# Kernel tuning notes

Measured on AMD Instinct MI355X. Metric: run time of the kernel, lower is better.

Reference implementation:

```python
import jax, jax.numpy as jnp
import numpy as np

D = 768
H = 16
DK = D // H
DFF = 3072
POOL = 100
NCLS = 7
EPS = 1e-6


def layer_norm(x, a, b):
    # torch: (x - mean) / (std + eps), std unbiased (ddof=1)
    mean = jnp.mean(x, axis=-1, keepdims=True)
    var = jnp.sum((x - mean) ** 2, axis=-1, keepdims=True) / (x.shape[-1] - 1)
    return a * (x - mean) / (jnp.sqrt(var) + EPS) + b


def mha(x, Wq, bq, Wk, bk, Wv, bv, Wo, bo):
    B, S, _ = x.shape
    def split(h):
        return h.reshape(B, S, H, DK).transpose(0, 2, 1, 3)  # [B,H,S,DK]
    q = split(x @ Wq + bq)
    k = split(x @ Wk + bk)
    v = split(x @ Wv + bv)
    scores = jnp.einsum('bhqd,bhkd->bhqk', q, k) / jnp.sqrt(jnp.float32(DK))
    p = jax.nn.softmax(scores, axis=-1)
    o = jnp.einsum('bhqk,bhkd->bhqd', p, v)
    o = o.transpose(0, 2, 1, 3).reshape(B, S, D)
    return o @ Wo + bo


def setup_inputs() -> dict:
    key = jax.random.key(0)
    ks = jax.random.split(key, 24)
    B, S = 8, 1023
    s = 0.02
    inp = {
        'text_features': jax.random.normal(ks[0], (B, S, D), jnp.float32),
        'prompt_pool': jax.random.normal(ks[1], (POOL, D), jnp.float32),
        'cls_token': jax.random.normal(ks[2], (1, 1, D), jnp.float32),
        'Wq': jax.random.normal(ks[3], (D, D), jnp.float32) * s,
        'bq': jnp.zeros((D,), jnp.float32),
        'Wk': jax.random.normal(ks[4], (D, D), jnp.float32) * s,
        'bk': jnp.zeros((D,), jnp.float32),
        'Wv': jax.random.normal(ks[5], (D, D), jnp.float32) * s,
        'bv': jnp.zeros((D,), jnp.float32),
        'Wo': jax.random.normal(ks[6], (D, D), jnp.float32) * s,
        'bo': jnp.zeros((D,), jnp.float32),
        'ln1_a': jnp.ones((D,), jnp.float32),
        'ln1_b': jnp.zeros((D,), jnp.float32),
        'ln2_a': jnp.ones((D,), jnp.float32),
        'ln2_b': jnp.zeros((D,), jnp.float32),
        'W1': jax.random.normal(ks[7], (D, DFF), jnp.float32) * s,
        'b1': jnp.zeros((DFF,), jnp.float32),
        'W2': jax.random.normal(ks[8], (DFF, D), jnp.float32) * s,
        'b2': jnp.zeros((D,), jnp.float32),
        'lnf_a': jnp.ones((D,), jnp.float32),
        'lnf_b': jnp.zeros((D,), jnp.float32),
        'Wpool': jax.random.normal(ks[9], (D, POOL), jnp.float32) * s,
        'bpool': jnp.zeros((POOL,), jnp.float32),
        'Wcls': jax.random.normal(ks[10], (D, NCLS), jnp.float32) * s,
        'bcls': jnp.zeros((NCLS,), jnp.float32),
    }
    return inp


def reference(text_features, prompt_pool, cls_token, Wq, bq, Wk, bk, Wv, bv, Wo, bo,
              ln1_a, ln1_b, ln2_a, ln2_b, W1, b1, W2, b2, lnf_a, lnf_b,
              Wpool, bpool, Wcls, bcls):
    B = text_features.shape[0]
    x = jnp.concatenate([jnp.broadcast_to(cls_token, (B, 1, D)), text_features], axis=1)
    # EncoderLayer (N=1), dropout in eval mode (identity)
    x = x + mha(layer_norm(x, ln1_a, ln1_b), Wq, bq, Wk, bk, Wv, bv, Wo, bo)
    h = layer_norm(x, ln2_a, ln2_b)
    x = x + (jax.nn.relu(h @ W1 + b1) @ W2 + b2)
    x = layer_norm(x, lnf_a, lnf_b)
    cls = x[:, 0, :]  # [B, D]
    probabilities = jax.nn.softmax(cls @ Wpool + bpool, axis=1)  # [B, POOL]
    class_logits = cls @ Wcls + bcls  # [B, NCLS]
    class_probs = jax.nn.softmax(class_logits, axis=1)
    entropy = -jnp.sum(class_probs * jnp.log(class_probs + 1e-9), axis=1)
    max_entropy = jnp.log(jnp.float32(7.0))
    norm_ent = entropy / max_entropy
    adjusted_k = jnp.clip(jnp.floor(1.0 + norm_ent * (POOL - 1)).astype(jnp.int32), 1, POOL)  # [B]
    # full descending top-k (jit-friendly: pad to POOL instead of data-dependent max_k)
    _, top_idx = jax.lax.top_k(probabilities, POOL)  # [B, POOL]
    gathered = prompt_pool[top_idx]  # [B, POOL, D]
    keep = (jnp.arange(POOL)[None, :] < adjusted_k[:, None]).astype(prompt_pool.dtype)
    selected_prompts = gathered * keep[:, :, None]
    return (selected_prompts, class_logits)
```

## Files before the change

### kernel.cpp

```cpp
#include <hip/hip_runtime.h>


#define OUT_CLS_OFF 614400

__device__ __forceinline__ float bsum256(float v, float* red) {
    int lane = threadIdx.x & 63, w = threadIdx.x >> 6;
#pragma unroll
    for (int off = 1; off < 64; off <<= 1) v += __shfl_xor(v, off);
    __syncthreads();
    if (lane == 0) red[w] = v;
    __syncthreads();
    return red[0] + red[1] + red[2] + red[3];
}
__device__ __forceinline__ float bmax256(float v, float* red) {
    int lane = threadIdx.x & 63, w = threadIdx.x >> 6;
#pragma unroll
    for (int off = 1; off < 64; off <<= 1) v = fmaxf(v, __shfl_xor(v, off));
    __syncthreads();
    if (lane == 0) red[w] = v;
    __syncthreads();
    return fmaxf(fmaxf(red[0], red[1]), fmaxf(red[2], red[3]));
}

__global__ __launch_bounds__(256) void q0_gemv(
    const float* __restrict__ clsT, const float* __restrict__ ga,
    const float* __restrict__ gb, const float* __restrict__ Wq,
    const float* __restrict__ bq, float* __restrict__ q0)
{
    __shared__ float ys[768];
    __shared__ float red[4];
    __shared__ float4 part[16][17];
    int t = threadIdx.x;
    float a0 = clsT[t], a1 = clsT[t + 256], a2 = clsT[t + 512];
    float mean = bsum256(a0 + a1 + a2, red) * (1.0f / 768.0f);
    float d0 = a0 - mean, d1 = a1 - mean, d2 = a2 - mean;
    float var = bsum256(d0 * d0 + d1 * d1 + d2 * d2, red) * (1.0f / 767.0f);
    float den = sqrtf(var) + 1e-6f;
    ys[t]       = (ga[t] * d0) / den + gb[t];
    ys[t + 256] = (ga[t + 256] * d1) / den + gb[t + 256];
    ys[t + 512] = (ga[t + 512] * d2) / den + gb[t + 512];
    __syncthreads();
    int c = blockIdx.x * 64 + (t & 15) * 4;
    int kq = t >> 4;
    float4 acc = {0.f, 0.f, 0.f, 0.f};
#pragma unroll 8
    for (int i = 0; i < 48; ++i) {
        int k = kq * 48 + i;
        float4 w = *(const float4*)&Wq[(size_t)k * 768 + c];
        float y = ys[k];
        acc.x = fmaf(y, w.x, acc.x); acc.y = fmaf(y, w.y, acc.y);
        acc.z = fmaf(y, w.z, acc.z); acc.w = fmaf(y, w.w, acc.w);
    }
    part[kq][t & 15] = acc;
    __syncthreads();
    if (t < 16) {
        float4 s = {0.f, 0.f, 0.f, 0.f};
#pragma unroll
        for (int i = 0; i < 16; ++i) {
            float4 v = part[i][t];
            s.x += v.x; s.y += v.y; s.z += v.z; s.w += v.w;
        }
        int cc = blockIdx.x * 64 + t * 4;
        float4 b4 = *(const float4*)&bq[cc];
        q0[cc] = s.x + b4.x; q0[cc + 1] = s.y + b4.y;
        q0[cc + 2] = s.z + b4.z; q0[cc + 3] = s.w + b4.w;
    }
}

__global__ __launch_bounds__(256) void wkq_prep(
    const float* __restrict__ Wk, const float* __restrict__ bk,
    const float* __restrict__ q0, float* __restrict__ wkqc)
{
    __shared__ float qs[768];
    int t = threadIdx.x;
    qs[t] = q0[t]; qs[t + 256] = q0[t + 256]; qs[t + 512] = q0[t + 512];
    __syncthreads();
    const float invs = 0.14433756729740643f;
    int kl = t >> 4, h = t & 15;
    int k = blockIdx.x * 16 + kl;
    const float* wr = Wk + (size_t)k * 768 + h * 48;
    const float* qh = qs + h * 48;
    float a = 0.f;
#pragma unroll
    for (int d = 0; d < 48; d += 4) {
        float4 w = *(const float4*)&wr[d];
        a += w.x * qh[d] + w.y * qh[d + 1] + w.z * qh[d + 2] + w.w * qh[d + 3];
    }
    wkqc[k * 16 + h] = a * invs;
    if (blockIdx.x == 0 && t < 16) {
        float c = 0.f;
        for (int d = 0; d < 48; ++d) c += bk[t * 48 + d] * qs[t * 48 + d];
        wkqc[12288 + t] = c * invs;
    }
}

__global__ __launch_bounds__(256) void wkq_consts(
    const float* __restrict__ ga, const float* __restrict__ gb,
    float* __restrict__ wkqc)
{
    __shared__ float pA[16][17], pB[16][17];
    int t = threadIdx.x;
    int h = t & 15, dg = t >> 4;
    float a = 0.f, bs = 0.f;
#pragma unroll 8
    for (int i = 0; i < 48; ++i) {
        int d = dg * 48 + i;
        float wv = wkqc[d * 16 + h];
        a = fmaf(ga[d], wv, a);
        bs = fmaf(gb[d], wv, bs);
    }
    pA[dg][h] = a; pB[dg][h] = bs;
    __syncthreads();
    if (t < 16) {
        float sa = 0.f, sb = 0.f;
#pragma unroll
        for (int i = 0; i < 16; ++i) { sa += pA[i][t]; sb += pB[i][t]; }
        wkqc[12304 + t] = sa;
        wkqc[12320 + t] = sb + wkqc[12288 + t];
    }
}

__global__ __launch_bounds__(256) void ln_scores(
    const float* __restrict__ tf, const float* __restrict__ clsT,
    const float* __restrict__ ga, const float* __restrict__ wkqc,
    float* __restrict__ sc, float2* __restrict__ stats)
{
    __shared__ float tr[256][17];
    __shared__ float partw[4][16];
    __shared__ float red[2][4][2];
    int t = threadIdx.x;
    int l = t & 63, w = t >> 6;

    float wk0[16], wk1[16], wk2[16];
    {
        const float4* p0 = (const float4*)(wkqc + t * 16);
        const float4* p1 = (const float4*)(wkqc + (t + 256) * 16);
        const float4* p2 = (const float4*)(wkqc + (t + 512) * 16);
#pragma unroll
        for (int q = 0; q < 4; ++q) {
            float4 v0 = p0[q], v1 = p1[q], v2 = p2[q];
            wk0[q * 4] = v0.x; wk0[q * 4 + 1] = v0.y; wk0[q * 4 + 2] = v0.z; wk0[q * 4 + 3] = v0.w;
            wk1[q * 4] = v1.x; wk1[q * 4 + 1] = v1.y; wk1[q * 4 + 2] = v1.z; wk1[q * 4 + 3] = v1.w;
            wk2[q * 4] = v2.x; wk2[q * 4 + 1] = v2.y; wk2[q * 4 + 2] = v2.z; wk2[q * 4 + 3] = v2.w;
        }
    }
    float ga0 = ga[t], ga1 = ga[t + 256], ga2 = ga[t + 512];
    float Sg = wkqc[12304 + (t & 15)];
    float Cg = wkqc[12320 + (t & 15)];

    int r0 = blockIdx.x * 8;
    for (int r = 0; r < 8; ++r) {
        int row = r0 + r;
        int b = row >> 10, j = row & 1023;
        const float* src = j ? (tf + ((size_t)b * 1023 + (j - 1)) * 768) : clsT;
        float x0 = src[t], x1 = src[t + 256], x2 = src[t + 512];
        float s1 = x0 + x1 + x2;
        float s2 = fmaf(x0, x0, fmaf(x1, x1, x2 * x2));
        float g0 = ga0 * x0, g1 = ga1 * x1, g2 = ga2 * x2;
        float dt[16];
#pragma unroll
        for (int h = 0; h < 16; ++h)
            dt[h] = fmaf(g0, wk0[h], fmaf(g1, wk1[h], g2 * wk2[h]));
#pragma unroll
        for (int off = 1; off < 64; off <<= 1) {
            s1 += __shfl_xor(s1, off);
            s2 += __shfl_xor(s2, off);
        }
        if (l == 0) { red[r & 1][w][0] = s1; red[r & 1][w][1] = s2; }
#pragma unroll
        for (int h = 0; h < 16; ++h) tr[t][h] = dt[h];
        __syncthreads();
        int hh = t & 15, ch = t >> 4;
        float v = 0.f;
#pragma unroll
        for (int i = 0; i < 16; ++i) v += tr[ch * 16 + i][hh];
        v += __shfl_xor(v, 16);
        v += __shfl_xor(v, 32);
        if (l < 16) partw[w][l] = v;
        __syncthreads();
        if (t < 16) {
            float dtot = partw[0][t] + partw[1][t] + partw[2][t] + partw[3][t];
            float s1t = red[r & 1][0][0] + red[r & 1][1][0] + red[r & 1][2][0] + red[r & 1][3][0];
            float s2t = red[r & 1][0][1] + red[r & 1][1][1] + red[r & 1][2][1] + red[r & 1][3][1];
            float mean = s1t * (1.0f / 768.0f);
            float var = (s2t - mean * s1t) * (1.0f / 767.0f);
            float rden = 1.0f / (sqrtf(var) + 1e-6f);
            float sv = rden * (dtot - mean * Sg) + Cg;
            sc[(((size_t)b * 16 + t) << 10) + j] = sv;
            if (t == 0) stats[row] = make_float2(mean, rden);
        }
    }
}

__global__ __launch_bounds__(256) void softmax_k(
    const float* __restrict__ sc, float* __restrict__ p)
{
    __shared__ float red[4];
    int bh = blockIdx.x, t = threadIdx.x;
    const float4* s4 = (const float4*)(sc + ((size_t)bh << 10));
    float4 v = s4[t];
    float m = fmaxf(fmaxf(v.x, v.y), fmaxf(v.z, v.w));
    float M = bmax256(m, red);
    float e0 = expf(v.x - M), e1 = expf(v.y - M), e2 = expf(v.z - M), e3 = expf(v.w - M);
    float Z = bsum256(e0 + e1 + e2 + e3, red);
    float4 o; o.x = e0 / Z; o.y = e1 / Z; o.z = e2 / Z; o.w = e3 / Z;
    ((float4*)(p + ((size_t)bh << 10)))[t] = o;
}

__global__ __launch_bounds__(256) void upart_k(
    const float* __restrict__ tf, const float* __restrict__ clsT,
    const float2* __restrict__ stats, const float* __restrict__ ga,
    const float* __restrict__ gb, const float* __restrict__ p,
    float* __restrict__ up)
{
    __shared__ float ps[16][32];
    int b = blockIdx.x & 7, jc = blockIdx.x >> 3;
    int t = threadIdx.x;
    if (t < 128) {
        int h = t >> 3, j4 = (t & 7) * 4;
        const float* prow = p + (((size_t)b * 16 + h) << 10) + jc * 32 + j4;
        float4 pv = *(const float4*)prow;
        ps[h][j4] = pv.x; ps[h][j4 + 1] = pv.y; ps[h][j4 + 2] = pv.z; ps[h][j4 + 3] = pv.w;
    }
    __syncthreads();
    float ga0 = ga[t], ga1 = ga[t + 256], ga2 = ga[t + 512];
    float gb0 = gb[t], gb1 = gb[t + 256], gb2 = gb[t + 512];
    float acc[16][3];
#pragma unroll
    for (int h = 0; h < 16; ++h) { acc[h][0] = 0.f; acc[h][1] = 0.f; acc[h][2] = 0.f; }

    int j0 = jc * 32;
    const float* s0p = j0 ? (tf + ((size_t)b * 1023 + (j0 - 1)) * 768) : clsT;
    float nx0 = s0p[t], nx1 = s0p[t + 256], nx2 = s0p[t + 512];
    float2 nst = stats[(b << 10) + j0];

    for (int jj = 0; jj < 32; ++jj) {
        float x0 = nx0, x1 = nx1, x2 = nx2;
        float2 st = nst;
        if (jj < 31) {
            int j2 = j0 + jj + 1;
            const float* sp = tf + ((size_t)b * 1023 + (j2 - 1)) * 768;
            nx0 = sp[t]; nx1 = sp[t + 256]; nx2 = sp[t + 512];
            nst = stats[(b << 10) + j2];
        }
        float xl0 = (ga0 * (x0 - st.x)) * st.y + gb0;
        float xl1 = (ga1 * (x1 - st.x)) * st.y + gb1;
        float xl2 = (ga2 * (x2 - st.x)) * st.y + gb2;
#pragma unroll
        for (int h = 0; h < 16; ++h) {
            float ph = ps[h][jj];
            acc[h][0] = fmaf(ph, xl0, acc[h][0]);
            acc[h][1] = fmaf(ph, xl1, acc[h][1]);
            acc[h][2] = fmaf(ph, xl2, acc[h][2]);
        }
    }
    float* o = up + (((size_t)b * 32 + jc) * 16) * 768;
#pragma unroll
    for (int h = 0; h < 16; ++h) {
        o[h * 768 + t] = acc[h][0];
        o[h * 768 + t + 256] = acc[h][1];
        o[h * 768 + t + 512] = acc[h][2];
    }
}

__global__ __launch_bounds__(256) void o0_k(
    const float* __restrict__ up, const float* __restrict__ Wv,
    const float* __restrict__ bv, float* __restrict__ o0)
{
    __shared__ float us[768];
    __shared__ float part[4][64];
    int h = blockIdx.x, b = blockIdx.y, t = threadIdx.x;
    float s0 = 0.f, s1 = 0.f, s2 = 0.f;
#pragma unroll 8
    for (int jc = 0; jc < 32; ++jc) {
        const float* q = up + (((size_t)b * 32 + jc) * 16 + h) * 768;
        s0 += q[t]; s1 += q[t + 256]; s2 += q[t + 512];
    }
    us[t] = s0; us[t + 256] = s1; us[t + 512] = s2;
    __syncthreads();
    int dd = t & 63, kg = t >> 6;
    float a = 0.f;
    if (dd < 48) {
#pragma unroll 8
        for (int i = 0; i < 192; ++i) {
            int k = kg * 192 + i;
            a = fmaf(us[k], Wv[(size_t)k * 768 + h * 48 + dd], a);
        }
    }
    part[kg][dd] = a;
    __syncthreads();
    if (t < 48)
        o0[(size_t)b * 768 + h * 48 + t] =
            part[0][t] + part[1][t] + part[2][t] + part[3][t] + bv[h * 48 + t];
}

__global__ __launch_bounds__(256) void x2_k(
    const float* __restrict__ o0, const float* __restrict__ Wo,
    const float* __restrict__ bo, const float* __restrict__ clsT,
    float* __restrict__ x2w)
{
    __shared__ float ys[768];
    __shared__ float4 part[16][17];
    int b = blockIdx.y, t = threadIdx.x;
    const float* xr = o0 + (size_t)b * 768;
    ys[t] = xr[t]; ys[t + 256] = xr[t + 256]; ys[t + 512] = xr[t + 512];
    __syncthreads();
    int c = blockIdx.x * 64 + (t & 15) * 4;
    int kq = t >> 4;
    float4 acc = {0.f, 0.f, 0.f, 0.f};
#pragma unroll 8
    for (int i = 0; i < 48; ++i) {
        int k = kq * 48 + i;
        float4 w = *(const float4*)&Wo[(size_t)k * 768 + c];
        float y = ys[k];
        acc.x = fmaf(y, w.x, acc.x); acc.y = fmaf(y, w.y, acc.y);
        acc.z = fmaf(y, w.z, acc.z); acc.w = fmaf(y, w.w, acc.w);
    }
    part[kq][t & 15] = acc;
    __syncthreads();
    if (t < 16) {
        float4 s = {0.f, 0.f, 0.f, 0.f};
#pragma unroll
        for (int i = 0; i < 16; ++i) {
            float4 v = part[i][t];
            s.x += v.x; s.y += v.y; s.z += v.z; s.w += v.w;
        }
        int cc = blockIdx.x * 64 + t * 4;
        float4 b4 = *(const float4*)&bo[cc];
        float4 r4 = *(const float4*)&clsT[cc];
        float* o = x2w + (size_t)b * 768 + cc;
        o[0] = s.x + b4.x + r4.x; o[1] = s.y + b4.y + r4.y;
        o[2] = s.z + b4.z + r4.z; o[3] = s.w + b4.w + r4.w;
    }
}

__global__ __launch_bounds__(256) void f1_k(
    const float* __restrict__ x2w, const float* __restrict__ ga,
    const float* __restrict__ gb, const float* __restrict__ W1,
    const float* __restrict__ b1, float* __restrict__ f1w)
{
    __shared__ float ys[768];
    __shared__ float red[4];
    __shared__ float4 part[8][33];
    int b = blockIdx.y, t = threadIdx.x;
    const float* xr = x2w + (size_t)b * 768;
    float a0 = xr[t], a1 = xr[t + 256], a2 = xr[t + 512];
    float mean = bsum256(a0 + a1 + a2, red) * (1.0f / 768.0f);
    float d0 = a0 - mean, d1 = a1 - mean, d2 = a2 - mean;
    float var = bsum256(d0 * d0 + d1 * d1 + d2 * d2, red) * (1.0f / 767.0f);
    float den = sqrtf(var) + 1e-6f;
    ys[t]       = (ga[t] * d0) / den + gb[t];
    ys[t + 256] = (ga[t + 256] * d1) / den + gb[t + 256];
    ys[t + 512] = (ga[t + 512] * d2) / den + gb[t + 512];
    __syncthreads();
    int c = blockIdx.x * 128 + (t & 31) * 4;
    int kq = t >> 5;
    float4 acc = {0.f, 0.f, 0.f, 0.f};
#pragma unroll 8
    for (int i = 0; i < 96; ++i) {
        int k = kq * 96 + i;
        float4 w = *(const float4*)&W1[(size_t)k * 3072 + c];
        float y = ys[k];
        acc.x = fmaf(y, w.x, acc.x); acc.y = fmaf(y, w.y, acc.y);
        acc.z = fmaf(y, w.z, acc.z); acc.w = fmaf(y, w.w, acc.w);
    }
    part[kq][t & 31] = acc;
    __syncthreads();
    if (t < 32) {
        float4 s = {0.f, 0.f, 0.f, 0.f};
#pragma unroll
        for (int i = 0; i < 8; ++i) {
            float4 v = part[i][t];
            s.x += v.x; s.y += v.y; s.z += v.z; s.w += v.w;
        }
        int cc = blockIdx.x * 128 + t * 4;
        float4 b4 = *(const float4*)&b1[cc];
        float* o = f1w + (size_t)b * 3072 + cc;
        o[0] = fmaxf(s.x + b4.x, 0.f); o[1] = fmaxf(s.y + b4.y, 0.f);
        o[2] = fmaxf(s.z + b4.z, 0.f); o[3] = fmaxf(s.w + b4.w, 0.f);
    }
}

__global__ __launch_bounds__(256) void x3_k(
    const float* __restrict__ f1w, const float* __restrict__ W2,
    const float* __restrict__ b2, const float* __restrict__ x2w,
    float* __restrict__ x3w)
{
    __shared__ float ys[3072];
    __shared__ float4 part[16][17];
    int b = blockIdx.y, t = threadIdx.x;
    const float* xr = f1w + (size_t)b * 3072;
    for (int i = t; i < 3072; i += 256) ys[i] = xr[i];
    __syncthreads();
    int c = blockIdx.x * 64 + (t & 15) * 4;
    int kq = t >> 4;
    float4 acc = {0.f, 0.f, 0.f, 0.f};
#pragma unroll 8
    for (int i = 0; i < 192; ++i) {
        int k = kq * 192 + i;
        float4 w = *(const float4*)&W2[(size_t)k * 768 + c];
        float y = ys[k];
        acc.x = fmaf(y, w.x, acc.x); acc.y = fmaf(y, w.y, acc.y);
        acc.z = fmaf(y, w.z, acc.z); acc.w = fmaf(y, w.w, acc.w);
    }
    part[kq][t & 15] = acc;
    __syncthreads();
    if (t < 16) {
        float4 s = {0.f, 0.f, 0.f, 0.f};
#pragma unroll
        for (int i = 0; i < 16; ++i) {
            float4 v = part[i][t];
            s.x += v.x; s.y += v.y; s.z += v.z; s.w += v.w;
        }
        int cc = blockIdx.x * 64 + t * 4;
        float4 b4 = *(const float4*)&b2[cc];
        const float* x2r = x2w + (size_t)b * 768 + cc;
        float* o = x3w + (size_t)b * 768 + cc;
        o[0] = x2r[0] + s.x + b4.x; o[1] = x2r[1] + s.y + b4.y;
        o[2] = x2r[2] + s.z + b4.z; o[3] = x2r[3] + s.w + b4.w;
    }
}

__global__ __launch_bounds__(256) void logits_part(
    const float* __restrict__ x3w, const float* __restrict__ ga,
    const float* __restrict__ gb, const float* __restrict__ Wpool,
    const float* __restrict__ Wcls, double* __restrict__ lp)
{
    __shared__ float ys[768];
    __shared__ float red[4];
    int kg = blockIdx.x, b = blockIdx.y, t = threadIdx.x;
    const float* xr = x3w + (size_t)b * 768;
    float a0 = xr[t], a1 = xr[t + 256], a2 = xr[t + 512];
    float mean = bsum256(a0 + a1 + a2, red) * (1.0f / 768.0f);
    float d0 = a0 - mean, d1 = a1 - mean, d2 = a2 - mean;
    float var = bsum256(d0 * d0 + d1 * d1 + d2 * d2, red) * (1.0f / 767.0f);
    float den = sqrtf(var) + 1e-6f;
    ys[t]       = (ga[t] * d0) / den + gb[t];
    ys[t + 256] = (ga[t + 256] * d1) / den + gb[t + 256];
    ys[t + 512] = (ga[t + 512] * d2) / den + gb[t + 512];
    __syncthreads();
    int kbase = kg * 96;
    if (t < 100) {
        double a = 0.0;
#pragma unroll 8
        for (int i = 0; i < 96; ++i) {
            int k = kbase + i;
            a = fma((double)ys[k], (double)Wpool[k * 100 + t], a);
        }
        lp[((size_t)b * 8 + kg) * 112 + t] = a;
    } else if (t < 107) {
        int c = t - 100;
        double a = 0.0;
#pragma unroll 8
        for (int i = 0; i < 96; ++i) {
            int k = kbase + i;
            a = fma((double)ys[k], (double)Wcls[k * 7 + c], a);
        }
        lp[((size_t)b * 8 + kg) * 112 + t] = a;
    }
}

__global__ __launch_bounds__(128) void head_decide(
    const double* __restrict__ lp, const float* __restrict__ bpool,
    const float* __restrict__ bcls, float* __restrict__ out,
    int* __restrict__ topw, int* __restrict__ kkw)
{
    __shared__ double sP[100];
    __shared__ double sC7[7];
    int b = blockIdx.x, t = threadIdx.x;
    if (t < 107) {
        double a = (t < 100) ? (double)bpool[t] : (double)bcls[t - 100];
#pragma unroll
        for (int kg = 0; kg < 8; ++kg) a += lp[((size_t)b * 8 + kg) * 112 + t];
        if (t < 100) sP[t] = a;
        else {
            sC7[t - 100] = a;
            out[OUT_CLS_OFF + b * 7 + (t - 100)] = (float)a;
        }
    }
    __syncthreads();
    double mx = sP[0];
    for (int j = 1; j < 100; ++j) mx = fmax(mx, sP[j]);
    double e = (t < 100) ? exp(sP[t] - mx) : 0.0;
    __syncthreads();
    if (t < 100) sP[t] = e;
    __syncthreads();
    double zs = 0.0;
    for (int j = 0; j < 100; ++j) zs += sP[j];
    __syncthreads();
    if (t < 100) sP[t] = e / zs;
    __syncthreads();
    if (t == 0) {
        double m7 = sC7[0];
        for (int j = 1; j < 7; ++j) m7 = fmax(m7, sC7[j]);
        double es[7]; double z = 0.0;
        for (int j = 0; j < 7; ++j) { es[j] = exp(sC7[j] - m7); z += es[j]; }
        double ent = 0.0;
        for (int j = 0; j < 7; ++j) { double pr = es[j] / z; ent -= pr * log(pr + 1e-9); }
        double ne = ent / log(7.0);
        int kk = (int)floor(1.0 + ne * 99.0);
        kkw[b] = kk < 1 ? 1 : (kk > 100 ? 100 : kk);
    }
    if (t < 100) {
        double pi = sP[t];
        int r = 0;
        for (int j = 0; j < 100; ++j) {
            double pj = sP[j];
            r += (pj > pi) || (pj == pi && j < t);
        }
        topw[b * 100 + r] = t;
    }
}

__global__ __launch_bounds__(192) void gather_k(
    const float* __restrict__ pool, const int* __restrict__ topw,
    const int* __restrict__ kkw, float* __restrict__ out)
{
    int r = blockIdx.x, b = blockIdx.y, t = threadIdx.x;
    int idx = topw[b * 100 + r];
    bool keep = r < kkw[b];
    const float4* src = (const float4*)(pool + (size_t)idx * 768);
    float4* dst = (float4*)(out + (size_t)b * 76800 + (size_t)r * 768);
    float4 z = {0.f, 0.f, 0.f, 0.f};
    dst[t] = keep ? src[t] : z;
}

extern "C" void kernel_launch(void* const* d_in, const int* in_sizes, int n_in,
                              void* d_out, int out_size, void* d_ws, size_t ws_size,
                              hipStream_t stream) {
    (void)in_sizes; (void)n_in; (void)out_size; (void)ws_size;
    const float* tf    = (const float*)d_in[0];
    const float* pool  = (const float*)d_in[1];
    const float* clsT  = (const float*)d_in[2];
    const float* Wq    = (const float*)d_in[3];
    const float* bq    = (const float*)d_in[4];
    const float* Wk    = (const float*)d_in[5];
    const float* bk    = (const float*)d_in[6];
    const float* Wv    = (const float*)d_in[7];
    const float* bv    = (const float*)d_in[8];
    const float* Wo    = (const float*)d_in[9];
    const float* bo    = (const float*)d_in[10];
    const float* ln1a  = (const float*)d_in[11];
    const float* ln1b  = (const float*)d_in[12];
    const float* ln2a  = (const float*)d_in[13];
    const float* ln2b  = (const float*)d_in[14];
    const float* W1    = (const float*)d_in[15];
    const float* b1    = (const float*)d_in[16];
    const float* W2    = (const float*)d_in[17];
    const float* b2    = (const float*)d_in[18];
    const float* lnfa  = (const float*)d_in[19];
    const float* lnfb  = (const float*)d_in[20];
    const float* Wpool = (const float*)d_in[21];
    const float* bpool = (const float*)d_in[22];
    const float* Wcls  = (const float*)d_in[23];
    const float* bcls  = (const float*)d_in[24];
    float* out = (float*)d_out;
    char* ws = (char*)d_ws;

    float*  sc    = (float*)(ws + 0);
    float*  p     = (float*)(ws + 524288);
    float2* stats = (float2*)(ws + 1048576);
    float*  wkqc  = (float*)(ws + 1114112);
    float*  q0    = (float*)(ws + 1163520);
    float*  upart = (float*)(ws + 1166592);
    float*  o0    = (float*)(ws + 13749504);
    float*  x2w   = (float*)(ws + 13774080);
    float*  f1w   = (float*)(ws + 13798656);
    float*  x3w   = (float*)(ws + 13896960);
    int*    topw  = (int*)(ws + 13921536);
    int*    kkw   = (int*)(ws + 13924736);
    double* lp    = (double*)(ws + 13924768);

    q0_gemv<<<12, 256, 0, stream>>>(clsT, ln1a, ln1b, Wq, bq, q0);
    wkq_prep<<<48, 256, 0, stream>>>(Wk, bk, q0, wkqc);
    wkq_consts<<<1, 256, 0, stream>>>(ln1a, ln1b, wkqc);
    ln_scores<<<1024, 256, 0, stream>>>(tf, clsT, ln1a, wkqc, sc, stats);
    softmax_k<<<128, 256, 0, stream>>>(sc, p);
    upart_k<<<256, 256, 0, stream>>>(tf, clsT, stats, ln1a, ln1b, p, upart);
    o0_k<<<dim3(16, 8), 256, 0, stream>>>(upart, Wv, bv, o0);
    x2_k<<<dim3(12, 8), 256, 0, stream>>>(o0, Wo, bo, clsT, x2w);
    f1_k<<<dim3(24, 8), 256, 0, stream>>>(x2w, ln2a, ln2b, W1, b1, f1w);
    x3_k<<<dim3(12, 8), 256, 0, stream>>>(f1w, W2, b2, x2w, x3w);
    logits_part<<<dim3(8, 8), 256, 0, stream>>>(x3w, lnfa, lnfb, Wpool, Wcls, lp);
    head_decide<<<8, 128, 0, stream>>>(lp, bpool, bcls, out, topw, kkw);
    gather_k<<<dim3(100, 8), 192, 0, stream>>>(pool, topw, kkw, out);
}
```

Baseline: 111.0 us.

## Fuse post-prep pipeline into one cooperative kernel with grid syncs

Replaces the chain of eleven kernels after the query prep with a single cooperative kernel of 256 blocks that runs each stage and separates them with grid.sync(). The aim is to remove per-launch overhead and tail gaps between many small kernels. It also folds the wkq_consts step into the prep kernels by precomputing ga·Wk and gb·Wk column sums, and prefetches the next row in the score and accumulation loops. In exchange the grid is limited to 256 blocks, so the row-heavy score stage does 32 rows per block instead of 8, and the large shared-memory footprint may limit occupancy.

New measurement: 365.0 us. 229% more time.

```diff
diff --git a/kernel.cpp b/kernel.cpp
--- a/kernel.cpp
+++ b/kernel.cpp
@@ -1,4 +1,7 @@
 #include <hip/hip_runtime.h>
+#include <hip/hip_cooperative_groups.h>
+
+namespace cg = cooperative_groups;
 
 
 #define OUT_CLS_OFF 614400
@@ -22,54 +25,88 @@
     return fmaxf(fmaxf(red[0], red[1]), fmaxf(red[2], red[3]));
 }
 
-__global__ __launch_bounds__(256) void q0_gemv(
+__global__ __launch_bounds__(256) void prep_a(
     const float* __restrict__ clsT, const float* __restrict__ ga,
     const float* __restrict__ gb, const float* __restrict__ Wq,
-    const float* __restrict__ bq, float* __restrict__ q0)
+    const float* __restrict__ bq, const float* __restrict__ Wk,
+    float* __restrict__ q0, float* __restrict__ colw)
 {
     __shared__ float ys[768];
     __shared__ float red[4];
-    __shared__ float4 part[16][17];
+    __shared__ float4 partA[16][17];
+    __shared__ float4 partB[16][17];
     int t = threadIdx.x;
-    float a0 = clsT[t], a1 = clsT[t + 256], a2 = clsT[t + 512];
-    float mean = bsum256(a0 + a1 + a2, red) * (1.0f / 768.0f);
-    float d0 = a0 - mean, d1 = a1 - mean, d2 = a2 - mean;
-    float var = bsum256(d0 * d0 + d1 * d1 + d2 * d2, red) * (1.0f / 767.0f);
-    float den = sqrtf(var) + 1e-6f;
-    ys[t]       = (ga[t] * d0) / den + gb[t];
-    ys[t + 256] = (ga[t + 256] * d1) / den + gb[t + 256];
-    ys[t + 512] = (ga[t + 512] * d2) / den + gb[t + 512];
-    __syncthreads();
-    int c = blockIdx.x * 64 + (t & 15) * 4;
-    int kq = t >> 4;
-    float4 acc = {0.f, 0.f, 0.f, 0.f};
-#pragma unroll 8
-    for (int i = 0; i < 48; ++i) {
-        int k = kq * 48 + i;
-        float4 w = *(const float4*)&Wq[(size_t)k * 768 + c];
-        float y = ys[k];
-        acc.x = fmaf(y, w.x, acc.x); acc.y = fmaf(y, w.y, acc.y);
-        acc.z = fmaf(y, w.z, acc.z); acc.w = fmaf(y, w.w, acc.w);
-    }
-    part[kq][t & 15] = acc;
-    __syncthreads();
-    if (t < 16) {
-        float4 s = {0.f, 0.f, 0.f, 0.f};
-#pragma unroll
-        for (int i = 0; i < 16; ++i) {
-            float4 v = part[i][t];
-            s.x += v.x; s.y += v.y; s.z += v.z; s.w += v.w;
-        }
-        int cc = blockIdx.x * 64 + t * 4;
-        float4 b4 = *(const float4*)&bq[cc];
-        q0[cc] = s.x + b4.x; q0[cc + 1] = s.y + b4.y;
-        q0[cc + 2] = s.z + b4.z; q0[cc + 3] = s.w + b4.w;
+    if (blockIdx.x < 12) {
+        float a0 = clsT[t], a1 = clsT[t + 256], a2 = clsT[t + 512];
+        float mean = bsum256(a0 + a1 + a2, red) * (1.0f / 768.0f);
+        float d0 = a0 - mean, d1 = a1 - mean, d2 = a2 - mean;
+        float var = bsum256(d0 * d0 + d1 * d1 + d2 * d2, red) * (1.0f / 767.0f);
+        float den = sqrtf(var) + 1e-6f;
+        ys[t]       = (ga[t] * d0) / den + gb[t];
+        ys[t + 256] = (ga[t + 256] * d1) / den + gb[t + 256];
+        ys[t + 512] = (ga[t + 512] * d2) / den + gb[t + 512];
+        __syncthreads();
+        int c = blockIdx.x * 64 + (t & 15) * 4;
+        int kq = t >> 4;
+        float4 acc = {0.f, 0.f, 0.f, 0.f};
+#pragma unroll 8
+        for (int i = 0; i < 48; ++i) {
+            int k = kq * 48 + i;
+            float4 w = *(const float4*)&Wq[(size_t)k * 768 + c];
+            float y = ys[k];
+            acc.x = fmaf(y, w.x, acc.x); acc.y = fmaf(y, w.y, acc.y);
+            acc.z = fmaf(y, w.z, acc.z); acc.w = fmaf(y, w.w, acc.w);
+        }
+        partA[kq][t & 15] = acc;
+        __syncthreads();
+        if (t < 16) {
+            float4 s = {0.f, 0.f, 0.f, 0.f};
+#pragma unroll
+            for (int i = 0; i < 16; ++i) {
+                float4 v = partA[i][t];
+                s.x += v.x; s.y += v.y; s.z += v.z; s.w += v.w;
+            }
+            int cc = blockIdx.x * 64 + t * 4;
+            float4 b4 = *(const float4*)&bq[cc];
+            q0[cc] = s.x + b4.x; q0[cc + 1] = s.y + b4.y;
+            q0[cc + 2] = s.z + b4.z; q0[cc + 3] = s.w + b4.w;
+        }
+    } else {
+        int c = (blockIdx.x - 12) * 64 + (t & 15) * 4;
+        int kq = t >> 4;
+        float4 aa = {0.f, 0.f, 0.f, 0.f}, ab = {0.f, 0.f, 0.f, 0.f};
+#pragma unroll 8
+        for (int i = 0; i < 48; ++i) {
+            int k = kq * 48 + i;
+            float4 w = *(const float4*)&Wk[(size_t)k * 768 + c];
+            float g = ga[k], h = gb[k];
+            aa.x = fmaf(g, w.x, aa.x); aa.y = fmaf(g, w.y, aa.y);
+            aa.z = fmaf(g, w.z, aa.z); aa.w = fmaf(g, w.w, aa.w);
+            ab.x = fmaf(h, w.x, ab.x); ab.y = fmaf(h, w.y, ab.y);
+            ab.z = fmaf(h, w.z, ab.z); ab.w = fmaf(h, w.w, ab.w);
+        }
+        partA[kq][t & 15] = aa;
+        partB[kq][t & 15] = ab;
+        __syncthreads();
+        if (t < 16) {
+            float4 sa = {0.f, 0.f, 0.f, 0.f}, sb = {0.f, 0.f, 0.f, 0.f};
+#pragma unroll
+            for (int i = 0; i < 16; ++i) {
+                float4 va = partA[i][t], vb = partB[i][t];
+                sa.x += va.x; sa.y += va.y; sa.z += va.z; sa.w += va.w;
+                sb.x += vb.x; sb.y += vb.y; sb.z += vb.z; sb.w += vb.w;
+            }
+            int cc = (blockIdx.x - 12) * 64 + t * 4;
+            *(float4*)&colw[cc] = sa;
+            *(float4*)&colw[768 + cc] = sb;
+        }
     }
 }
 
-__global__ __launch_bounds__(256) void wkq_prep(
+__global__ __launch_bounds__(256) void prep_b(
     const float* __restrict__ Wk, const float* __restrict__ bk,
-    const float* __restrict__ q0, float* __restrict__ wkqc)
+    const float* __restrict__ q0, const float* __restrict__ colw,
+    float* __restrict__ wkqc)
 {
     __shared__ float qs[768];
     int t = threadIdx.x;
@@ -88,51 +125,56 @@
     }
     wkqc[k * 16 + h] = a * invs;
     if (blockIdx.x == 0 && t < 16) {
-        float c = 0.f;
-        for (int d = 0; d < 48; ++d) c += bk[t * 48 + d] * qs[t * 48 + d];
-        wkqc[12288 + t] = c * invs;
+        float cd = 0.f, sa = 0.f, sb = 0.f;
+        for (int d = 0; d < 48; ++d) {
+            int dd = t * 48 + d;
+            cd = fmaf(bk[dd], qs[dd], cd);
+            sa = fmaf(colw[dd], qs[dd], sa);
+            sb = fmaf(colw[768 + dd], qs[dd], sb);
+        }
+        wkqc[12304 + t] = sa * invs;
+        wkqc[12320 + t] = sb * invs + cd * invs;
     }
 }
 
-__global__ __launch_bounds__(256) void wkq_consts(
-    const float* __restrict__ ga, const float* __restrict__ gb,
-    float* __restrict__ wkqc)
+__global__ __launch_bounds__(256) void fused_k(
+    const float* __restrict__ tf, const float* __restrict__ clsT,
+    const float* __restrict__ ln1a, const float* __restrict__ ln1b,
+    const float* __restrict__ wkqc, float* __restrict__ sc,
+    float2* __restrict__ stats, float* __restrict__ qb,
+    float* __restrict__ c1w, float* __restrict__ up,
+    const float* __restrict__ Wv, const float* __restrict__ bv,
+    float* __restrict__ o0, const float* __restrict__ Wo,
+    const float* __restrict__ bo, float* __restrict__ x2w,
+    const float* __restrict__ ln2a, const float* __restrict__ ln2b,
+    const float* __restrict__ W1, const float* __restrict__ b1,
+    float* __restrict__ f1w, const float* __restrict__ W2,
+    const float* __restrict__ b2, float* __restrict__ x3w,
+    const float* __restrict__ lnfa, const float* __restrict__ lnfb,
+    const float* __restrict__ Wpool, const float* __restrict__ Wcls,
+    double* __restrict__ lp, const float* __restrict__ bpool,
+    const float* __restrict__ bcls, const float* __restrict__ pool,
+    float* __restrict__ out, int* __restrict__ topw, int* __restrict__ kkw)
 {
-    __shared__ float pA[16][17], pB[16][17];
-    int t = threadIdx.x;
-    int h = t & 15, dg = t >> 4;
-    float a = 0.f, bs = 0.f;
-#pragma unroll 8
-    for (int i = 0; i < 48; ++i) {
-        int d = dg * 48 + i;
-        float wv = wkqc[d * 16 + h];
-        a = fmaf(ga[d], wv, a);
-        bs = fmaf(gb[d], wv, bs);
-    }
-    pA[dg][h] = a; pB[dg][h] = bs;
-    __syncthreads();
-    if (t < 16) {
-        float sa = 0.f, sb = 0.f;
-#pragma unroll
-        for (int i = 0; i < 16; ++i) { sa += pA[i][t]; sb += pB[i][t]; }
-        wkqc[12304 + t] = sa;
-        wkqc[12320 + t] = sb + wkqc[12288 + t];
-    }
-}
-
-__global__ __launch_bounds__(256) void ln_scores(
-    const float* __restrict__ tf, const float* __restrict__ clsT,
-    const float* __restrict__ ga, const float* __restrict__ wkqc,
-    float* __restrict__ sc, float2* __restrict__ stats)
-{
+    cg::grid_group grid = cg::this_grid();
     __shared__ float tr[256][17];
     __shared__ float partw[4][16];
-    __shared__ float red[2][4][2];
-    int t = threadIdx.x;
-    int l = t & 63, w = t >> 6;
-
-    float wk0[16], wk1[16], wk2[16];
+    __shared__ float redw[2][4][2];
+    __shared__ float red[4];
+    __shared__ float qs_s[16][32];
+    __shared__ float us[768];
+    __shared__ float part64[4][64];
+    __shared__ float ys[3072];
+    __shared__ float4 part16[16][17];
+    __shared__ float4 part8[8][33];
+    __shared__ double sPd[100];
+    __shared__ double sC7d[7];
+
+    const int bid = blockIdx.x, t = threadIdx.x;
+    const int l = t & 63, w = t >> 6;
+
     {
+        float wk0[16], wk1[16], wk2[16];
         const float4* p0 = (const float4*)(wkqc + t * 16);
         const float4* p1 = (const float4*)(wkqc + (t + 256) * 16);
         const float4* p2 = (const float4*)(wkqc + (t + 512) * 16);
@@ -143,386 +185,352 @@
             wk1[q * 4] = v1.x; wk1[q * 4 + 1] = v1.y; wk1[q * 4 + 2] = v1.z; wk1[q * 4 + 3] = v1.w;
             wk2[q * 4] = v2.x; wk2[q * 4 + 1] = v2.y; wk2[q * 4 + 2] = v2.z; wk2[q * 4 + 3] = v2.w;
         }
-    }
-    float ga0 = ga[t], ga1 = ga[t + 256], ga2 = ga[t + 512];
-    float Sg = wkqc[12304 + (t & 15)];
-    float Cg = wkqc[12320 + (t & 15)];
-
-    int r0 = blockIdx.x * 8;
-    for (int r = 0; r < 8; ++r) {
-        int row = r0 + r;
-        int b = row >> 10, j = row & 1023;
-        const float* src = j ? (tf + ((size_t)b * 1023 + (j - 1)) * 768) : clsT;
-        float x0 = src[t], x1 = src[t + 256], x2 = src[t + 512];
-        float s1 = x0 + x1 + x2;
-        float s2 = fmaf(x0, x0, fmaf(x1, x1, x2 * x2));
-        float g0 = ga0 * x0, g1 = ga1 * x1, g2 = ga2 * x2;
-        float dt[16];
-#pragma unroll
-        for (int h = 0; h < 16; ++h)
-            dt[h] = fmaf(g0, wk0[h], fmaf(g1, wk1[h], g2 * wk2[h]));
-#pragma unroll
-        for (int off = 1; off < 64; off <<= 1) {
-            s1 += __shfl_xor(s1, off);
-            s2 += __shfl_xor(s2, off);
-        }
-        if (l == 0) { red[r & 1][w][0] = s1; red[r & 1][w][1] = s2; }
-#pragma unroll
-        for (int h = 0; h < 16; ++h) tr[t][h] = dt[h];
-        __syncthreads();
-        int hh = t & 15, ch = t >> 4;
-        float v = 0.f;
-#pragma unroll
-        for (int i = 0; i < 16; ++i) v += tr[ch * 16 + i][hh];
-        v += __shfl_xor(v, 16);
-        v += __shfl_xor(v, 32);
-        if (l < 16) partw[w][l] = v;
+        float ga0 = ln1a[t], ga1 = ln1a[t + 256], ga2 = ln1a[t + 512];
+        float Sgv = wkqc[12304 + (t & 15)];
+        float Cgv = wkqc[12320 + (t & 15)];
+        int b = bid >> 5;
+        int j0 = (bid & 31) * 32;
+        const float* sp0 = j0 ? (tf + ((size_t)b * 1023 + (j0 - 1)) * 768) : clsT;
+        float nx0 = sp0[t], nx1 = sp0[t + 256], nx2 = sp0[t + 512];
+        for (int r = 0; r < 32; ++r) {
+            int j = j0 + r;
+            float x0 = nx0, x1 = nx1, x2 = nx2;
+            if (r < 31) {
+                const float* sp = tf + ((size_t)b * 1023 + j) * 768;
+                nx0 = sp[t]; nx1 = sp[t + 256]; nx2 = sp[t + 512];
+            }
+            float s1 = x0 + x1 + x2;
+            float s2 = fmaf(x0, x0, fmaf(x1, x1, x2 * x2));
+            float g0 = ga0 * x0, g1 = ga1 * x1, g2 = ga2 * x2;
+            float dt[16];
+#pragma unroll
+            for (int h = 0; h < 16; ++h)
+                dt[h] = fmaf(g0, wk0[h], fmaf(g1, wk1[h], g2 * wk2[h]));
+#pragma unroll
+            for (int off = 1; off < 64; off <<= 1) {
+                s1 += __shfl_xor(s1, off);
+                s2 += __shfl_xor(s2, off);
+            }
+            if (l == 0) { redw[r & 1][w][0] = s1; redw[r & 1][w][1] = s2; }
+#pragma unroll
+            for (int h = 0; h < 16; ++h) tr[t][h] = dt[h];
+            __syncthreads();
+            int hh = t & 15, ch = t >> 4;
+            float v = 0.f;
+#pragma unroll
+            for (int i = 0; i < 16; ++i) v += tr[ch * 16 + i][hh];
+            v += __shfl_xor(v, 16);
+            v += __shfl_xor(v, 32);
+            if (l < 16) partw[w][l] = v;
+            __syncthreads();
+            if (t < 16) {
+                float dtot = partw[0][t] + partw[1][t] + partw[2][t] + partw[3][t];
+                float s1t = redw[r & 1][0][0] + redw[r & 1][1][0] + redw[r & 1][2][0] + redw[r & 1][3][0];
+                float s2t = redw[r & 1][0][1] + redw[r & 1][1][1] + redw[r & 1][2][1] + redw[r & 1][3][1];
+                float mean = s1t * (1.0f / 768.0f);
+                float var = (s2t - mean * s1t) * (1.0f / 767.0f);
+                float rden = 1.0f / (sqrtf(var) + 1e-6f);
+                sc[(((size_t)b * 16 + t) << 10) + j] = rden * (dtot - mean * Sgv) + Cgv;
+                if (t == 0) stats[(b << 10) + j] = make_float2(mean, rden);
+            }
+        }
+    }
+    grid.sync();
+
+    if (bid < 128) {
+        int b = bid >> 4;
+        const float4* s4 = (const float4*)(sc + ((size_t)bid << 10));
+        float4 v = s4[t];
+        float m = fmaxf(fmaxf(v.x, v.y), fmaxf(v.z, v.w));
+        float M = bmax256(m, red);
+        float e0 = expf(v.x - M), e1 = expf(v.y - M), e2 = expf(v.z - M), e3 = expf(v.w - M);
+        float Z = bsum256(e0 + e1 + e2 + e3, red);
+        float2 st0 = stats[(b << 10) + 4 * t];
+        float2 st1 = stats[(b << 10) + 4 * t + 1];
+        float2 st2 = stats[(b << 10) + 4 * t + 2];
+        float2 st3 = stats[(b << 10) + 4 * t + 3];
+        float q0v = (e0 / Z) * st0.y, q1v = (e1 / Z) * st1.y;
+        float q2v = (e2 / Z) * st2.y, q3v = (e3 / Z) * st3.y;
+        float c1p = q0v * st0.x + q1v * st1.x + q2v * st2.x + q3v * st3.x;
+        float c1t = bsum256(c1p, red);
+        float4 o4; o4.x = q0v; o4.y = q1v; o4.z = q2v; o4.w = q3v;
+        ((float4*)(qb + ((size_t)bid << 10)))[t] = o4;
+        if (t == 0) c1w[bid] = c1t;
+    }
+    grid.sync();
+
+    {
+        int b = bid & 7, jc = bid >> 3;
+        if (t < 128) {
+            int h = t >> 3, j4 = (t & 7) * 4;
+            float4 pv = *(const float4*)(qb + (((size_t)b * 16 + h) << 10) + jc * 32 + j4);
+            qs_s[h][j4] = pv.x; qs_s[h][j4 + 1] = pv.y;
+            qs_s[h][j4 + 2] = pv.z; qs_s[h][j4 + 3] = pv.w;
+        }
+        __syncthreads();
+        float acc[16][3];
+#pragma unroll
+        for (int h = 0; h < 16; ++h) { acc[h][0] = 0.f; acc[h][1] = 0.f; acc[h][2] = 0.f; }
+        int j0 = jc * 32;
+        const float* sp0 = j0 ? (tf + ((size_t)b * 1023 + (j0 - 1)) * 768) : clsT;
+        float nx0 = sp0[t], nx1 = sp0[t + 256], nx2 = sp0[t + 512];
+        for (int jj = 0; jj < 32; ++jj) {
+            float x0 = nx0, x1 = nx1, x2 = nx2;
+            if (jj < 31) {
+                const float* sp = tf + ((size_t)b * 1023 + j0 + jj) * 768;
+                nx0 = sp[t]; nx1 = sp[t + 256]; nx2 = sp[t + 512];
+            }
+#pragma unroll
+            for (int h = 0; h < 16; ++h) {
+                float qh = qs_s[h][jj];
+                acc[h][0] = fmaf(qh, x0, acc[h][0]);
+                acc[h][1] = fmaf(qh, x1, acc[h][1]);
+                acc[h][2] = fmaf(qh, x2, acc[h][2]);
+            }
+        }
+        float* o = up + (((size_t)b * 32 + jc) * 16) * 768;
+#pragma unroll
+        for (int h = 0; h < 16; ++h) {
+            o[h * 768 + t] = acc[h][0];
+            o[h * 768 + t + 256] = acc[h][1];
+            o[h * 768 + t + 512] = acc[h][2];
+        }
+    }
+    grid.sync();
+
+    if (bid < 128) {
+        int h = bid & 15, b = bid >> 4;
+        float s0 = 0.f, s1 = 0.f, s2 = 0.f;
+#pragma unroll 8
+        for (int jc = 0; jc < 32; ++jc) {
+            const float* q = up + (((size_t)b * 32 + jc) * 16 + h) * 768;
+            s0 += q[t]; s1 += q[t + 256]; s2 += q[t + 512];
+        }
+        float c1 = c1w[b * 16 + h];
+        us[t]       = ln1a[t] * (s0 - c1) + ln1b[t];
+        us[t + 256] = ln1a[t + 256] * (s1 - c1) + ln1b[t + 256];
+        us[t + 512] = ln1a[t + 512] * (s2 - c1) + ln1b[t + 512];
+        __syncthreads();
+        int dd = t & 63, kg = t >> 6;
+        float a = 0.f;
+        if (dd < 48) {
+#pragma unroll 8
+            for (int i = 0; i < 192; ++i) {
+                int k = kg * 192 + i;
+                a = fmaf(us[k], Wv[(size_t)k * 768 + h * 48 + dd], a);
+            }
+        }
+        part64[kg][dd] = a;
+        __syncthreads();
+        if (t < 48)
+            o0[(size_t)b * 768 + h * 48 + t] =
+                part64[0][t] + part64[1][t] + part64[2][t] + part64[3][t] + bv[h * 48 + t];
+    }
+    grid.sync();
+
+    if (bid < 96) {
+        int cb = bid >> 3, b = bid & 7;
+        const float* xr = o0 + (size_t)b * 768;
+        ys[t] = xr[t]; ys[t + 256] = xr[t + 256]; ys[t + 512] = xr[t + 512];
+        __syncthreads();
+        int c = cb * 64 + (t & 15) * 4;
+        int kq = t >> 4;
+        float4 acc = {0.f, 0.f, 0.f, 0.f};
+#pragma unroll 8
+        for (int i = 0; i < 48; ++i) {
+            int k = kq * 48 + i;
+            float4 wv = *(const float4*)&Wo[(size_t)k * 768 + c];
+            float y = ys[k];
+            acc.x = fmaf(y, wv.x, acc.x); acc.y = fmaf(y, wv.y, acc.y);
+            acc.z = fmaf(y, wv.z, acc.z); acc.w = fmaf(y, wv.w, acc.w);
+        }
+        part16[kq][t & 15] = acc;
         __syncthreads();
         if (t < 16) {
-            float dtot = partw[0][t] + partw[1][t] + partw[2][t] + partw[3][t];
-            float s1t = red[r & 1][0][0] + red[r & 1][1][0] + red[r & 1][2][0] + red[r & 1][3][0];
-            float s2t = red[r & 1][0][1] + red[r & 1][1][1] + red[r & 1][2][1] + red[r & 1][3][1];
-            float mean = s1t * (1.0f / 768.0f);
-            float var = (s2t - mean * s1t) * (1.0f / 767.0f);
-            float rden = 1.0f / (sqrtf(var) + 1e-6f);
-            float sv = rden * (dtot - mean * Sg) + Cg;
-            sc[(((size_t)b * 16 + t) << 10) + j] = sv;
-            if (t == 0) stats[row] = make_float2(mean, rden);
-        }
-    }
-}
-
-__global__ __launch_bounds__(256) void softmax_k(
-    const float* __restrict__ sc, float* __restrict__ p)
-{
-    __shared__ float red[4];
-    int bh = blockIdx.x, t = threadIdx.x;
-    const float4* s4 = (const float4*)(sc + ((size_t)bh << 10));
-    float4 v = s4[t];
-    float m = fmaxf(fmaxf(v.x, v.y), fmaxf(v.z, v.w));
-    float M = bmax256(m, red);
-    float e0 = expf(v.x - M), e1 = expf(v.y - M), e2 = expf(v.z - M), e3 = expf(v.w - M);
-    float Z = bsum256(e0 + e1 + e2 + e3, red);
-    float4 o; o.x = e0 / Z; o.y = e1 / Z; o.z = e2 / Z; o.w = e3 / Z;
-    ((float4*)(p + ((size_t)bh << 10)))[t] = o;
-}
-
-__global__ __launch_bounds__(256) void upart_k(
-    const float* __restrict__ tf, const float* __restrict__ clsT,
-    const float2* __restrict__ stats, const float* __restrict__ ga,
-    const float* __restrict__ gb, const float* __restrict__ p,
-    float* __restrict__ up)
-{
-    __shared__ float ps[16][32];
-    int b = blockIdx.x & 7, jc = blockIdx.x >> 3;
-    int t = threadIdx.x;
-    if (t < 128) {
-        int h = t >> 3, j4 = (t & 7) * 4;
-        const float* prow = p + (((size_t)b * 16 + h) << 10) + jc * 32 + j4;
-        float4 pv = *(const float4*)prow;
-        ps[h][j4] = pv.x; ps[h][j4 + 1] = pv.y; ps[h][j4 + 2] = pv.z; ps[h][j4 + 3] = pv.w;
-    }
-    __syncthreads();
-    float ga0 = ga[t], ga1 = ga[t + 256], ga2 = ga[t + 512];
-    float gb0 = gb[t], gb1 = gb[t + 256], gb2 = gb[t + 512];
-    float acc[16][3];
-#pragma unroll
-    for (int h = 0; h < 16; ++h) { acc[h][0] = 0.f; acc[h][1] = 0.f; acc[h][2] = 0.f; }
-
-    int j0 = jc * 32;
-    const float* s0p = j0 ? (tf + ((size_t)b * 1023 + (j0 - 1)) * 768) : clsT;
-    float nx0 = s0p[t], nx1 = s0p[t + 256], nx2 = s0p[t + 512];
-    float2 nst = stats[(b << 10) + j0];
-
-    for (int jj = 0; jj < 32; ++jj) {
-        float x0 = nx0, x1 = nx1, x2 = nx2;
-        float2 st = nst;
-        if (jj < 31) {
-            int j2 = j0 + jj + 1;
-            const float* sp = tf + ((size_t)b * 1023 + (j2 - 1)) * 768;
-            nx0 = sp[t]; nx1 = sp[t + 256]; nx2 = sp[t + 512];
-            nst = stats[(b << 10) + j2];
-        }
-        float xl0 = (ga0 * (x0 - st.x)) * st.y + gb0;
-        float xl1 = (ga1 * (x1 - st.x)) * st.y + gb1;
-        float xl2 = (ga2 * (x2 - st.x)) * st.y + gb2;
-#pragma unroll
-        for (int h = 0; h < 16; ++h) {
-            float ph = ps[h][jj];
-            acc[h][0] = fmaf(ph, xl0, acc[h][0]);
-            acc[h][1] = fmaf(ph, xl1, acc[h][1]);
-            acc[h][2] = fmaf(ph, xl2, acc[h][2]);
-        }
-    }
-    float* o = up + (((size_t)b * 32 + jc) * 16) * 768;
-#pragma unroll
-    for (int h = 0; h < 16; ++h) {
-        o[h * 768 + t] = acc[h][0];
-        o[h * 768 + t + 256] = acc[h][1];
-        o[h * 768 + t + 512] = acc[h][2];
-    }
-}
-
-__global__ __launch_bounds__(256) void o0_k(
-    const float* __restrict__ up, const float* __restrict__ Wv,
-    const float* __restrict__ bv, float* __restrict__ o0)
-{
-    __shared__ float us[768];
-    __shared__ float part[4][64];
-    int h = blockIdx.x, b = blockIdx.y, t = threadIdx.x;
-    float s0 = 0.f, s1 = 0.f, s2 = 0.f;
-#pragma unroll 8
-    for (int jc = 0; jc < 32; ++jc) {
-        const float* q = up + (((size_t)b * 32 + jc) * 16 + h) * 768;
-        s0 += q[t]; s1 += q[t + 256]; s2 += q[t + 512];
-    }
-    us[t] = s0; us[t + 256] = s1; us[t + 512] = s2;
-    __syncthreads();
-    int dd = t & 63, kg = t >> 6;
-    float a = 0.f;
-    if (dd < 48) {
+            float4 s = {0.f, 0.f, 0.f, 0.f};
+#pragma unroll
+            for (int i = 0; i < 16; ++i) {
+                float4 v = part16[i][t];
+                s.x += v.x; s.y += v.y; s.z += v.z; s.w += v.w;
+            }
+            int cc = cb * 64 + t * 4;
+            float4 b4 = *(const float4*)&bo[cc];
+            float4 r4 = *(const float4*)&clsT[cc];
+            float* o = x2w + (size_t)b * 768 + cc;
+            o[0] = s.x + b4.x + r4.x; o[1] = s.y + b4.y + r4.y;
+            o[2] = s.z + b4.z + r4.z; o[3] = s.w + b4.w + r4.w;
+        }
+    }
+    grid.sync();
+
+    if (bid < 192) {
+        int cb = bid >> 3, b = bid & 7;
+        const float* xr = x2w + (size_t)b * 768;
+        float a0 = xr[t], a1 = xr[t + 256], a2 = xr[t + 512];
+        float mean = bsum256(a0 + a1 + a2, red) * (1.0f / 768.0f);
+        float d0 = a0 - mean, d1 = a1 - mean, d2 = a2 - mean;
+        float var = bsum256(d0 * d0 + d1 * d1 + d2 * d2, red) * (1.0f / 767.0f);
+        float den = sqrtf(var) + 1e-6f;
+        ys[t]       = (ln2a[t] * d0) / den + ln2b[t];
+        ys[t + 256] = (ln2a[t + 256] * d1) / den + ln2b[t + 256];
+        ys[t + 512] = (ln2a[t + 512] * d2) / den + ln2b[t + 512];
+        __syncthreads();
+        int c = cb * 128 + (t & 31) * 4;
+        int kq = t >> 5;
+        float4 acc = {0.f, 0.f, 0.f, 0.f};
+#pragma unroll 8
+        for (int i = 0; i < 96; ++i) {
+            int k = kq * 96 + i;
+            float4 wv = *(const float4*)&W1[(size_t)k * 3072 + c];
+            float y = ys[k];
+            acc.x = fmaf(y, wv.x, acc.x); acc.y = fmaf(y, wv.y, acc.y);
+            acc.z = fmaf(y, wv.z, acc.z); acc.w = fmaf(y, wv.w, acc.w);
+        }
+        part8[kq][t & 31] = acc;
+        __syncthreads();
+        if (t < 32) {
+            float4 s = {0.f, 0.f, 0.f, 0.f};
+#pragma unroll
+            for (int i = 0; i < 8; ++i) {
+                float4 v = part8[i][t];
+                s.x += v.x; s.y += v.y; s.z += v.z; s.w += v.w;
+            }
+            int cc = cb * 128 + t * 4;
+            float4 b4 = *(const float4*)&b1[cc];
+            float* o = f1w + (size_t)b * 3072 + cc;
+            o[0] = fmaxf(s.x + b4.x, 0.f); o[1] = fmaxf(s.y + b4.y, 0.f);
+            o[2] = fmaxf(s.z + b4.z, 0.f); o[3] = fmaxf(s.w + b4.w, 0.f);
+        }
+    }
+    grid.sync();
+
+    if (bid < 96) {
+        int cb = bid >> 3, b = bid & 7;
+        const float* xr = f1w + (size_t)b * 3072;
+        for (int i = t; i < 3072; i += 256) ys[i] = xr[i];
+        __syncthreads();
+        int c = cb * 64 + (t & 15) * 4;
+        int kq = t >> 4;
+        float4 acc = {0.f, 0.f, 0.f, 0.f};
 #pragma unroll 8
         for (int i = 0; i < 192; ++i) {
-            int k = kg * 192 + i;
-            a = fmaf(us[k], Wv[(size_t)k * 768 + h * 48 + dd], a);
-        }
-    }
-    part[kg][dd] = a;
-    __syncthreads();
-    if (t < 48)
-        o0[(size_t)b * 768 + h * 48 + t] =
-            part[0][t] + part[1][t] + part[2][t] + part[3][t] + bv[h * 48 + t];
-}
-
-__global__ __launch_bounds__(256) void x2_k(
-    const float* __restrict__ o0, const float* __restrict__ Wo,
-    const float* __restrict__ bo, const float* __restrict__ clsT,
-    float* __restrict__ x2w)
-{
-    __shared__ float ys[768];
-    __shared__ float4 part[16][17];
-    int b = blockIdx.y, t = threadIdx.x;
-    const float* xr = o0 + (size_t)b * 768;
-    ys[t] = xr[t]; ys[t + 256] = xr[t + 256]; ys[t + 512] = xr[t + 512];
-    __syncthreads();
-    int c = blockIdx.x * 64 + (t & 15) * 4;
-    int kq = t >> 4;
-    float4 acc = {0.f, 0.f, 0.f, 0.f};
-#pragma unroll 8
-    for (int i = 0; i < 48; ++i) {
-        int k = kq * 48 + i;
-        float4 w = *(const float4*)&Wo[(size_t)k * 768 + c];
-        float y = ys[k];
-        acc.x = fmaf(y, w.x, acc.x); acc.y = fmaf(y, w.y, acc.y);
-        acc.z = fmaf(y, w.z, acc.z); acc.w = fmaf(y, w.w, acc.w);
-    }
-    part[kq][t & 15] = acc;
-    __syncthreads();
-    if (t < 16) {
-        float4 s = {0.f, 0.f, 0.f, 0.f};
-#pragma unroll
-        for (int i = 0; i < 16; ++i) {
-            float4 v = part[i][t];
-            s.x += v.x; s.y += v.y; s.z += v.z; s.w += v.w;
-        }
-        int cc = blockIdx.x * 64 + t * 4;
-        float4 b4 = *(const float4*)&bo[cc];
-        float4 r4 = *(const float4*)&clsT[cc];
-        float* o = x2w + (size_t)b * 768 + cc;
-        o[0] = s.x + b4.x + r4.x; o[1] = s.y + b4.y + r4.y;
-        o[2] = s.z + b4.z + r4.z; o[3] = s.w + b4.w + r4.w;
-    }
-}
-
-__global__ __launch_bounds__(256) void f1_k(
-    const float* __restrict__ x2w, const float* __restrict__ ga,
-    const float* __restrict__ gb, const float* __restrict__ W1,
-    const float* __restrict__ b1, float* __restrict__ f1w)
-{
-    __shared__ float ys[768];
-    __shared__ float red[4];
-    __shared__ float4 part[8][33];
-    int b = blockIdx.y, t = threadIdx.x;
-    const float* xr = x2w + (size_t)b * 768;
-    float a0 = xr[t], a1 = xr[t + 256], a2 = xr[t + 512];
-    float mean = bsum256(a0 + a1 + a2, red) * (1.0f / 768.0f);
-    float d0 = a0 - mean, d1 = a1 - mean, d2 = a2 - mean;
-    float var = bsum256(d0 * d0 + d1 * d1 + d2 * d2, red) * (1.0f / 767.0f);
-    float den = sqrtf(var) + 1e-6f;
-    ys[t]       = (ga[t] * d0) / den + gb[t];
-    ys[t + 256] = (ga[t + 256] * d1) / den + gb[t + 256];
-    ys[t + 512] = (ga[t + 512] * d2) / den + gb[t + 512];
-    __syncthreads();
-    int c = blockIdx.x * 128 + (t & 31) * 4;
-    int kq = t >> 5;
-    float4 acc = {0.f, 0.f, 0.f, 0.f};
-#pragma unroll 8
-    for (int i = 0; i < 96; ++i) {
-        int k = kq * 96 + i;
-        float4 w = *(const float4*)&W1[(size_t)k * 3072 + c];
-        float y = ys[k];
-        acc.x = fmaf(y, w.x, acc.x); acc.y = fmaf(y, w.y, acc.y);
-        acc.z = fmaf(y, w.z, acc.z); acc.w = fmaf(y, w.w, acc.w);
-    }
-    part[kq][t & 31] = acc;
-    __syncthreads();
-    if (t < 32) {
-        float4 s = {0.f, 0.f, 0.f, 0.f};
-#pragma unroll
-        for (int i = 0; i < 8; ++i) {
-            float4 v = part[i][t];
-            s.x += v.x; s.y += v.y; s.z += v.z; s.w += v.w;
-        }
-        int cc = blockIdx.x * 128 + t * 4;
-        float4 b4 = *(const float4*)&b1[cc];
-        float* o = f1w + (size_t)b * 3072 + cc;
-        o[0] = fmaxf(s.x + b4.x, 0.f); o[1] = fmaxf(s.y + b4.y, 0.f);
-        o[2] = fmaxf(s.z + b4.z, 0.f); o[3] = fmaxf(s.w + b4.w, 0.f);
-    }
-}
-
-__global__ __launch_bounds__(256) void x3_k(
-    const float* __restrict__ f1w, const float* __restrict__ W2,
-    const float* __restrict__ b2, const float* __restrict__ x2w,
-    float* __restrict__ x3w)
-{
-    __shared__ float ys[3072];
-    __shared__ float4 part[16][17];
-    int b = blockIdx.y, t = threadIdx.x;
-    const float* xr = f1w + (size_t)b * 3072;
-    for (int i = t; i < 3072; i += 256) ys[i] = xr[i];
-    __syncthreads();
-    int c = blockIdx.x * 64 + (t & 15) * 4;
-    int kq = t >> 4;
-    float4 acc = {0.f, 0.f, 0.f, 0.f};
-#pragma unroll 8
-    for (int i = 0; i < 192; ++i) {
-        int k = kq * 192 + i;
-        float4 w = *(const float4*)&W2[(size_t)k * 768 + c];
-        float y = ys[k];
-        acc.x = fmaf(y, w.x, acc.x); acc.y = fmaf(y, w.y, acc.y);
-        acc.z = fmaf(y, w.z, acc.z); acc.w = fmaf(y, w.w, acc.w);
-    }
-    part[kq][t & 15] = acc;
-    __syncthreads();
-    if (t < 16) {
-        float4 s = {0.f, 0.f, 0.f, 0.f};
-#pragma unroll
-        for (int i = 0; i < 16; ++i) {
-            float4 v = part[i][t];
-            s.x += v.x; s.y += v.y; s.z += v.z; s.w += v.w;
-        }
-        int cc = blockIdx.x * 64 + t * 4;
-        float4 b4 = *(const float4*)&b2[cc];
-        const float* x2r = x2w + (size_t)b * 768 + cc;
-        float* o = x3w + (size_t)b * 768 + cc;
-        o[0] = x2r[0] + s.x + b4.x; o[1] = x2r[1] + s.y + b4.y;
-        o[2] = x2r[2] + s.z + b4.z; o[3] = x2r[3] + s.w + b4.w;
-    }
-}
-
-__global__ __launch_bounds__(256) void logits_part(
-    const float* __restrict__ x3w, const float* __restrict__ ga,
-    const float* __restrict__ gb, const float* __restrict__ Wpool,
-    const float* __restrict__ Wcls, double* __restrict__ lp)
-{
-    __shared__ float ys[768];
-    __shared__ float red[4];
-    int kg = blockIdx.x, b = blockIdx.y, t = threadIdx.x;
-    const float* xr = x3w + (size_t)b * 768;
-    float a0 = xr[t], a1 = xr[t + 256], a2 = xr[t + 512];
-    float mean = bsum256(a0 + a1 + a2, red) * (1.0f / 768.0f);
-    float d0 = a0 - mean, d1 = a1 - mean, d2 = a2 - mean;
-    float var = bsum256(d0 * d0 + d1 * d1 + d2 * d2, red) * (1.0f / 767.0f);
-    float den = sqrtf(var) + 1e-6f;
-    ys[t]       = (ga[t] * d0) / den + gb[t];
-    ys[t + 256] = (ga[t + 256] * d1) / den + gb[t + 256];
-    ys[t + 512] = (ga[t + 512] * d2) / den + gb[t + 512];
-    __syncthreads();
-    int kbase = kg * 96;
-    if (t < 100) {
-        double a = 0.0;
-#pragma unroll 8
-        for (int i = 0; i < 96; ++i) {
-            int k = kbase + i;
-            a = fma((double)ys[k], (double)Wpool[k * 100 + t], a);
-        }
-        lp[((size_t)b * 8 + kg) * 112 + t] = a;
-    } else if (t < 107) {
-        int c = t - 100;
-        double a = 0.0;
-#pragma unroll 8
-        for (int i = 0; i < 96; ++i) {
-            int k = kbase + i;
-            a = fma((double)ys[k], (double)Wcls[k * 7 + c], a);
-        }
-        lp[((size_t)b * 8 + kg) * 112 + t] = a;
-    }
-}
-
-__global__ __launch_bounds__(128) void head_decide(
-    const double* __restrict__ lp, const float* __restrict__ bpool,
-    const float* __restrict__ bcls, float* __restrict__ out,
-    int* __restrict__ topw, int* __restrict__ kkw)
-{
-    __shared__ double sP[100];
-    __shared__ double sC7[7];
-    int b = blockIdx.x, t = threadIdx.x;
-    if (t < 107) {
-        double a = (t < 100) ? (double)bpool[t] : (double)bcls[t - 100];
-#pragma unroll
-        for (int kg = 0; kg < 8; ++kg) a += lp[((size_t)b * 8 + kg) * 112 + t];
-        if (t < 100) sP[t] = a;
-        else {
-            sC7[t - 100] = a;
-            out[OUT_CLS_OFF + b * 7 + (t - 100)] = (float)a;
-        }
-    }
-    __syncthreads();
-    double mx = sP[0];
-    for (int j = 1; j < 100; ++j) mx = fmax(mx, sP[j]);
-    double e = (t < 100) ? exp(sP[t] - mx) : 0.0;
-    __syncthreads();
-    if (t < 100) sP[t] = e;
-    __syncthreads();
-    double zs = 0.0;
-    for (int j = 0; j < 100; ++j) zs += sP[j];
-    __syncthreads();
-    if (t < 100) sP[t] = e / zs;
-    __syncthreads();
-    if (t == 0) {
-        double m7 = sC7[0];
-        for (int j = 1; j < 7; ++j) m7 = fmax(m7, sC7[j]);
-        double es[7]; double z = 0.0;
-        for (int j = 0; j < 7; ++j) { es[j] = exp(sC7[j] - m7); z += es[j]; }
-        double ent = 0.0;
-        for (int j = 0; j < 7; ++j) { double pr = es[j] / z; ent -= pr * log(pr + 1e-9); }
-        double ne = ent / log(7.0);
-        int kk = (int)floor(1.0 + ne * 99.0);
-        kkw[b] = kk < 1 ? 1 : (kk > 100 ? 100 : kk);
-    }
-    if (t < 100) {
-        double pi = sP[t];
-        int r = 0;
-        for (int j = 0; j < 100; ++j) {
-            double pj = sP[j];
-            r += (pj > pi) || (pj == pi && j < t);
-        }
-        topw[b * 100 + r] = t;
-    }
-}
-
-__global__ __launch_bounds__(192) void gather_k(
-    const float* __restrict__ pool, const int* __restrict__ topw,
-    const int* __restrict__ kkw, float* __restrict__ out)
-{
-    int r = blockIdx.x, b = blockIdx.y, t = threadIdx.x;
-    int idx = topw[b * 100 + r];
-    bool keep = r < kkw[b];
-    const float4* src = (const float4*)(pool + (size_t)idx * 768);
-    float4* dst = (float4*)(out + (size_t)b * 76800 + (size_t)r * 768);
-    float4 z = {0.f, 0.f, 0.f, 0.f};
-    dst[t] = keep ? src[t] : z;
+            int k = kq * 192 + i;
+            float4 wv = *(const float4*)&W2[(size_t)k * 768 + c];
+            float y = ys[k];
+            acc.x = fmaf(y, wv.x, acc.x); acc.y = fmaf(y, wv.y, acc.y);
+            acc.z = fmaf(y, wv.z, acc.z); acc.w = fmaf(y, wv.w, acc.w);
+        }
+        part16[kq][t & 15] = acc;
+        __syncthreads();
+        if (t < 16) {
+            float4 s = {0.f, 0.f, 0.f, 0.f};
+#pragma unroll
+            for (int i = 0; i < 16; ++i) {
+                float4 v = part16[i][t];
+                s.x += v.x; s.y += v.y; s.z += v.z; s.w += v.w;
+            }
+            int cc = cb * 64 + t * 4;
+            float4 b4 = *(const float4*)&b2[cc];
+            const float* x2r = x2w + (size_t)b * 768 + cc;
+            float* o = x3w + (size_t)b * 768 + cc;
+            o[0] = x2r[0] + s.x + b4.x; o[1] = x2r[1] + s.y + b4.y;
+            o[2] = x2r[2] + s.z + b4.z; o[3] = x2r[3] + s.w + b4.w;
+        }
+    }
+    grid.sync();
+
+    if (bid < 64) {
+        int kg = bid >> 3, b = bid & 7;
+        const float* xr = x3w + (size_t)b * 768;
+        float a0 = xr[t], a1 = xr[t + 256], a2 = xr[t + 512];
+        float mean = bsum256(a0 + a1 + a2, red) * (1.0f / 768.0f);
+        float d0 = a0 - mean, d1 = a1 - mean, d2 = a2 - mean;
+        float var = bsum256(d0 * d0 + d1 * d1 + d2 * d2, red) * (1.0f / 767.0f);
+        float den = sqrtf(var) + 1e-6f;
+        ys[t]       = (lnfa[t] * d0) / den + lnfb[t];
+        ys[t + 256] = (lnfa[t + 256] * d1) / den + lnfb[t + 256];
+        ys[t + 512] = (lnfa[t + 512] * d2) / den + lnfb[t + 512];
+        __syncthreads();
+        int kbase = kg * 96;
+        if (t < 100) {
+            double a = 0.0;
+#pragma unroll 8
+            for (int i = 0; i < 96; ++i) {
+                int k = kbase + i;
+                a = fma((double)ys[k], (double)Wpool[k * 100 + t], a);
+            }
+            lp[((size_t)b * 8 + kg) * 112 + t] = a;
+        } else if (t < 107) {
+            int c = t - 100;
+            double a = 0.0;
+#pragma unroll 8
+            for (int i = 0; i < 96; ++i) {
+                int k = kbase + i;
+                a = fma((double)ys[k], (double)Wcls[k * 7 + c], a);
+            }
+            lp[((size_t)b * 8 + kg) * 112 + t] = a;
+        }
+    }
+    grid.sync();
+
+    if (bid < 8) {
+        int b = bid;
+        if (t < 107) {
+            double a = (t < 100) ? (double)bpool[t] : (double)bcls[t - 100];
+#pragma unroll
+            for (int kg = 0; kg < 8; ++kg) a += lp[((size_t)b * 8 + kg) * 112 + t];
+            if (t < 100) sPd[t] = a;
+            else {
+                sC7d[t - 100] = a;
+                out[OUT_CLS_OFF + b * 7 + (t - 100)] = (float)a;
+            }
+        }
+        __syncthreads();
+        double mx = sPd[0];
+        for (int j = 1; j < 100; ++j) mx = fmax(mx, sPd[j]);
+        double e = (t < 100) ? exp(sPd[t] - mx) : 0.0;
+        __syncthreads();
+        if (t < 100) sPd[t] = e;
+        __syncthreads();
+        double zs = 0.0;
+        for (int j = 0; j < 100; ++j) zs += sPd[j];
+        __syncthreads();
+        if (t < 100) sPd[t] = e / zs;
+        __syncthreads();
+        if (t == 0) {
+            double m7 = sC7d[0];
+            for (int j = 1; j < 7; ++j) m7 = fmax(m7, sC7d[j]);
+            double es[7]; double z = 0.0;
+            for (int j = 0; j < 7; ++j) { es[j] = exp(sC7d[j] - m7); z += es[j]; }
+            double ent = 0.0;
+            for (int j = 0; j < 7; ++j) { double pr = es[j] / z; ent -= pr * log(pr + 1e-9); }
+            double ne = ent / log(7.0);
+            int kk = (int)floor(1.0 + ne * 99.0);
+            kkw[b] = kk < 1 ? 1 : (kk > 100 ? 100 : kk);
+        }
+        if (t < 100) {
+            double pi = sPd[t];
+            int r = 0;
+            for (int j = 0; j < 100; ++j) {
+                double pj = sPd[j];
+                r += (pj > pi) || (pj == pi && j < t);
+            }
+            topw[b * 100 + r] = t;
+        }
+    }
+    grid.sync();
+
+    for (int i = bid; i < 800; i += 256) {
+        int b = i & 7, r = i >> 3;
+        int idx = topw[b * 100 + r];
+        bool keep = r < kkw[b];
+        if (t < 192) {
+            const float4* src = (const float4*)(pool + (size_t)idx * 768);
+            float4* dst = (float4*)(out + (size_t)b * 76800 + (size_t)r * 768);
+            float4 z = {0.f, 0.f, 0.f, 0.f};
+            dst[t] = keep ? src[t] : z;
+        }
+    }
 }
 
 extern "C" void kernel_launch(void* const* d_in, const int* in_sizes, int n_in,
@@ -558,30 +566,28 @@
     char* ws = (char*)d_ws;
 
     float*  sc    = (float*)(ws + 0);
-    float*  p     = (float*)(ws + 524288);
+    float*  qb    = (float*)(ws + 524288);
     float2* stats = (float2*)(ws + 1048576);
     float*  wkqc  = (float*)(ws + 1114112);
     float*  q0    = (float*)(ws + 1163520);
-    float*  upart = (float*)(ws + 1166592);
-    float*  o0    = (float*)(ws + 13749504);
-    float*  x2w   = (float*)(ws + 13774080);
-    float*  f1w   = (float*)(ws + 13798656);
-    float*  x3w   = (float*)(ws + 13896960);
-    int*    topw  = (int*)(ws + 13921536);
-    int*    kkw   = (int*)(ws + 13924736);
-    double* lp    = (double*)(ws + 13924768);
-
-    q0_gemv<<<12, 256, 0, stream>>>(clsT, ln1a, ln1b, Wq, bq, q0);
-    wkq_prep<<<48, 256, 0, stream>>>(Wk, bk, q0, wkqc);
-    wkq_consts<<<1, 256, 0, stream>>>(ln1a, ln1b, wkqc);
-    ln_scores<<<1024, 256, 0, stream>>>(tf, clsT, ln1a, wkqc, sc, stats);
-    softmax_k<<<128, 256, 0, stream>>>(sc, p);
-    upart_k<<<256, 256, 0, stream>>>(tf, clsT, stats, ln1a, ln1b, p, upart);
-    o0_k<<<dim3(16, 8), 256, 0, stream>>>(upart, Wv, bv, o0);
-    x2_k<<<dim3(12, 8), 256, 0, stream>>>(o0, Wo, bo, clsT, x2w);
-    f1_k<<<dim3(24, 8), 256, 0, stream>>>(x2w, ln2a, ln2b, W1, b1, f1w);
-    x3_k<<<dim3(12, 8), 256, 0, stream>>>(f1w, W2, b2, x2w, x3w);
-    logits_part<<<dim3(8, 8), 256, 0, stream>>>(x3w, lnfa, lnfb, Wpool, Wcls, lp);
-    head_decide<<<8, 128, 0, stream>>>(lp, bpool, bcls, out, topw, kkw);
-    gather_k<<<dim3(100, 8), 192, 0, stream>>>(pool, topw, kkw, out);
+    float*  colw  = (float*)(ws + 1166592);
+    float*  c1w   = (float*)(ws + 1172736);
+    float*  up    = (float*)(ws + 1173248);
+    float*  o0    = (float*)(ws + 13756160);
+    float*  x2w   = (float*)(ws + 13780736);
+    float*  f1w   = (float*)(ws + 13805312);
+    float*  x3w   = (float*)(ws + 13903616);
+    int*    topw  = (int*)(ws + 13928192);
+    int*    kkw   = (int*)(ws + 13931392);
+    double* lp    = (double*)(ws + 13931424);
+
+    prep_a<<<24, 256, 0, stream>>>(clsT, ln1a, ln1b, Wq, bq, Wk, q0, colw);
+    prep_b<<<48, 256, 0, stream>>>(Wk, bk, q0, colw, wkqc);
+
+    void* ka[] = { &tf, &clsT, &ln1a, &ln1b, &wkqc, &sc, &stats, &qb, &c1w, &up,
+                   &Wv, &bv, &o0, &Wo, &bo, &x2w, &ln2a, &ln2b, &W1, &b1, &f1w,
+                   &W2, &b2, &x3w, &lnfa, &lnfb, &Wpool, &Wcls, &lp, &bpool,
+                   &bcls, &pool, &out, &topw, &kkw };
+    hipLaunchCooperativeKernel(reinterpret_cast<void*>(fused_k),
+                               dim3(256), dim3(256), ka, 0, stream);
 }
```
